# Kernel tuning notes

Measured on AMD Instinct MI355X. Metric: run time of the kernel, lower is better.

The kernel has to match this reference:

```python
import jax, jax.numpy as jnp
import numpy as np
from jax import lax

M_POINT = 1024
NSAMPLE = 16
GRASPNESS_THRESHOLD = 0.1
HMIN, HMAX = -0.02, 0.04  # cylinder height range (GraspNet CloudCrop)
RADII = (0.025, 0.05, 0.075, 0.1)
BIG = 1e10


def _fps(xyz, mask):
    """Masked furthest point sampling. xyz [N,3], mask [N] bool -> idx [M_POINT] int32.
    Masked-out points carry -BIG min-distance so they are never selected."""
    first = jnp.argmax(mask).astype(jnp.int32)  # first graspable point (ragged FPS start)
    dists = jnp.where(mask, BIG, -BIG)
    idxs = jnp.zeros((M_POINT,), jnp.int32).at[0].set(first)

    def body(i, carry):
        idxs, dists = carry
        last = xyz[idxs[i - 1]]
        d = jnp.sum((xyz - last) ** 2, axis=-1)
        dists = jnp.where(mask, jnp.minimum(dists, d), -BIG)
        nxt = jnp.argmax(dists).astype(jnp.int32)
        return idxs.at[i].set(nxt), dists

    idxs, _ = lax.fori_loop(1, M_POINT, body, (idxs, dists))
    return idxs


def _cylinder_crop(xyz_g, feat_g, rot, radius, w1, b1, w2, b2):
    """Cylinder query + group + shared MLP + maxpool.
    xyz_g [B,M,3], feat_g [B,M,C], rot [B,M,3,3] -> [B,M,256]."""
    B, M, _ = xyz_g.shape
    # offsets of candidate n relative to seed m, expressed in the seed's gripper frame
    diff = xyz_g[:, None, :, :] - xyz_g[:, :, None, :]          # [B,M(seed),M(cand),3]
    local = jnp.einsum('bmnj,bmji->bmni', diff, rot)            # rotate into approach frame
    along = local[..., 0]
    r2 = local[..., 1] ** 2 + local[..., 2] ** 2
    cond = (r2 < radius * radius) & (along > HMIN) & (along < HMAX)  # [B,M,M]
    # first NSAMPLE in-cylinder indices (ball-query semantics: pad with first hit)
    order = jnp.where(cond, jnp.arange(M)[None, None, :], M)
    sel = jnp.argsort(order, axis=-1)[..., :NSAMPLE].astype(jnp.int32)  # [B,M,NS]
    cnt = cond.sum(axis=-1)                                     # [B,M]
    fill = sel[..., :1]
    idx = jnp.where(jnp.arange(NSAMPLE)[None, None, :] < cnt[..., None], sel, fill)
    idx = jnp.where(cnt[..., None] > 0, idx, 0)
    grouped_xyz = jnp.take_along_axis(local, idx[..., None], axis=2) / radius  # [B,M,NS,3]
    grouped_feat = feat_g[jnp.arange(B)[:, None, None], idx]                    # [B,M,NS,C]
    g = jnp.concatenate([grouped_xyz, grouped_feat], axis=-1)                   # [B,M,NS,3+C]
    h = jax.nn.relu(jnp.einsum('bmnf,of->bmno', g, w1) + b1)
    h = jax.nn.relu(jnp.einsum('bmnf,of->bmno', h, w2) + b2)
    return h.max(axis=2)                                                        # [B,M,256]


def setup_inputs() -> dict:
    key = jax.random.key(0)
    ks = jax.random.split(key, 10)
    B, N, C = 4, 20000, 512
    return {
        'seed_xyz': jax.random.normal(ks[0], (B, N, 3), jnp.float32),
        'seed_features': jax.random.normal(ks[1], (B, C, N), jnp.float32),
        'objectness_score': jax.random.normal(ks[2], (B, 2, N), jnp.float32),
        'graspness_score': jax.random.uniform(ks[3], (B, N), jnp.float32),
        'grasp_top_views_rot': jax.random.normal(ks[4], (B, M_POINT, 3, 3), jnp.float32),
        'crop_w1': jax.random.normal(ks[5], (4, 256, 3 + C), jnp.float32) * 0.05,
        'crop_b1': jnp.zeros((4, 256), jnp.float32),
        'crop_w2': jax.random.normal(ks[6], (4, 256, 256), jnp.float32) * 0.05,
        'crop_b2': jnp.zeros((4, 256), jnp.float32),
        'fuse_w': jax.random.normal(ks[7], (256, 1024), jnp.float32) * 0.05,
        'fuse_b': jnp.zeros((256,), jnp.float32),
    }


def reference(seed_xyz, seed_features, objectness_score, graspness_score,
              grasp_top_views_rot, crop_w1, crop_b1, crop_w2, crop_b2,
              fuse_w, fuse_b):
    # graspable mask (per-point, data dependent)
    objectness_mask = jnp.argmax(objectness_score, axis=1) == 1       # [B,N]
    graspness_mask = graspness_score > GRASPNESS_THRESHOLD
    graspable_mask = objectness_mask & graspness_mask
    # masked FPS per sample, then gather
    idxs = jax.vmap(_fps)(seed_xyz, graspable_mask)                    # [B,M]
    xyz_g = jnp.take_along_axis(seed_xyz, idxs[:, :, None], axis=1)    # [B,M,3]
    feat = seed_features.transpose(0, 2, 1)                            # [B,N,C]
    feat_g = jnp.take_along_axis(feat, idxs[:, :, None], axis=1)       # [B,M,C]
    # multiscale cylinder crops
    feats = [_cylinder_crop(xyz_g, feat_g, grasp_top_views_rot, RADII[k],
                            crop_w1[k], crop_b1[k], crop_w2[k], crop_b2[k])
             for k in range(4)]
    cat = jnp.concatenate(feats, axis=-1)                              # [B,M,1024]
    fused = jnp.einsum('bmf,of->bom', cat, fuse_w) + fuse_b[None, :, None]  # [B,256,M]
    return fused
```

## Files before the change

### kernel.cpp

```cpp
#include <hip/hip_runtime.h>
#include <cstdint>
#include <cfloat>
#include <climits>

#define NPTS 20000
#define NB 4
#define MP 1024
#define CF 512
#define MAXCH 20
#define KFAST 10240
#define PPT 20

__constant__ float c_r2[4]  = { (float)(0.025*0.025), (float)(0.05*0.05),
                                (float)(0.075*0.075), (float)(0.1*0.1) };
__constant__ float c_rad[4] = { 0.025f, 0.05f, 0.075f, 0.1f };

#define DPP_XOR1   0xB1
#define DPP_XOR2   0x4E
#define DPP_HMIRR  0x141
#define DPP_MIRR   0x140
#define DPP_BC15   0x142
#define DPP_BC31   0x143

template<int CTRL>
__device__ __forceinline__ unsigned long long kmax_step(unsigned long long k)
{
    unsigned int lo = (unsigned int)k;
    unsigned int hi = (unsigned int)(k >> 32);
    unsigned int olo = (unsigned int)__builtin_amdgcn_update_dpp((int)lo, (int)lo, CTRL, 0xf, 0xf, false);
    unsigned int ohi = (unsigned int)__builtin_amdgcn_update_dpp((int)hi, (int)hi, CTRL, 0xf, 0xf, false);
    unsigned long long ok = ((unsigned long long)ohi << 32) | (unsigned long long)olo;
    return (ok > k) ? ok : k;
}

__global__ __launch_bounds__(1024)
void k_fps_compact(const float* __restrict__ xyz, const float* __restrict__ obj,
                   const float* __restrict__ grasp,
                   float* __restrict__ xc, float* __restrict__ yc,
                   float* __restrict__ zc, int* __restrict__ ci,
                   int* __restrict__ kv)
{
    const int b = blockIdx.x;
    const int tid = threadIdx.x;
    const int lane = tid & 63, wid = tid >> 6;
    const float* xb  = xyz   + (size_t)b * NPTS * 3;
    const float* ob0 = obj   + (size_t)b * 2 * NPTS;
    const float* ob1 = ob0 + NPTS;
    const float* gb  = grasp + (size_t)b * NPTS;
    float* xcb = xc + (size_t)b * 20480;
    float* ycb = yc + (size_t)b * 20480;
    float* zcb = zc + (size_t)b * 20480;
    int*   cib = ci + (size_t)b * 20480;

    __shared__ int sWaveCnt[16];

    int kbase = 0;
    for (int i = 0; i < MAXCH; ++i) {
        int n = i * MP + tid;
        bool msk = false; float x = 0.f, y = 0.f, z = 0.f;
        if (n < NPTS) {
            msk = (ob1[n] > ob0[n]) && (gb[n] > 0.1f);
            if (msk) { x = xb[n*3+0]; y = xb[n*3+1]; z = xb[n*3+2]; }
        }
        unsigned long long bal = __ballot(msk);
        if (lane == 0) sWaveCnt[wid] = __popcll(bal);
        __syncthreads();
        int pre = 0, tot = 0;
        for (int w = 0; w < 16; ++w) { int c = sWaveCnt[w]; tot += c; if (w < wid) pre += c; }
        if (msk) {
            int rank = kbase + pre + __popcll(bal & ((1ull << lane) - 1ull));
            xcb[rank] = x; ycb[rank] = y; zcb[rank] = z; cib[rank] = n;
        }
        kbase += tot;
        __syncthreads();
    }
    if (tid == 0) kv[b] = kbase;
}

__global__ __launch_bounds__(512, 2)
void k_fps_loop(const float* __restrict__ xyz, const int* __restrict__ kv,
                const float* __restrict__ xc, const float* __restrict__ yc,
                const float* __restrict__ zc, const int* __restrict__ ci,
                int* __restrict__ idxs, float* __restrict__ xyz_g)
{
    const int b = blockIdx.x;
    const int tid = threadIdx.x;
    const int lane = tid & 63, wid = tid >> 6;
    const float* xb  = xyz + (size_t)b * NPTS * 3;
    const float* xcb = xc + (size_t)b * 20480;
    const float* ycb = yc + (size_t)b * 20480;
    const float* zcb = zc + (size_t)b * 20480;
    const int*   cib = ci + (size_t)b * 20480;

    __shared__ float sXYZ[3 * KFAST];
    __shared__ int   s_sel[MP];
    __shared__ unsigned long long sKy[2][8];
    float* sX = sXYZ;
    float* sY = sXYZ + KFAST;
    float* sZ = sXYZ + 2 * KFAST;

    const int K = kv[b];

    if (K == 0) {
        for (int t = tid; t < MP; t += 512) {
            idxs[b*MP + t] = 0;
            xyz_g[((size_t)b*MP + t)*3 + 0] = xb[0];
            xyz_g[((size_t)b*MP + t)*3 + 1] = xb[1];
            xyz_g[((size_t)b*MP + t)*3 + 2] = xb[2];
        }
        return;
    }

    if (K <= KFAST) {
        for (int c = tid; c < KFAST; c += 512) {
            bool v = c < K;
            sX[c] = v ? xcb[c] : 0.f;
            sY[c] = v ? ycb[c] : 0.f;
            sZ[c] = v ? zcb[c] : 0.f;
        }
        __syncthreads();

        float px[PPT], py[PPT], pz[PPT], pd[PPT];
#pragma unroll
        for (int i = 0; i < PPT; ++i) {
            int c = tid + (i << 9);
            px[i] = sX[c]; py[i] = sY[c]; pz[i] = sZ[c];
            pd[i] = (c < K) ? 1e10f : -3.0e38f;
        }
        float lx = sX[0], ly = sY[0], lz = sZ[0];
        if (tid == 0) s_sel[0] = 0;

        for (int it = 1; it < MP; ++it) {
            const int p = it & 1;
#pragma unroll
            for (int i = 0; i < PPT; ++i) {
                float dx = px[i] - lx, dy = py[i] - ly, dz = pz[i] - lz;
                float d = __fadd_rn(__fadd_rn(__fmul_rn(dx,dx), __fmul_rn(dy,dy)),
                                    __fmul_rn(dz,dz));
                pd[i] = fminf(pd[i], d);
            }
            float gv[5]; int gi[5];
#pragma unroll
            for (int g = 0; g < 5; ++g) {
                const int i0 = g * 4;
                bool t0 = pd[i0+1] > pd[i0+0];
                float v01 = t0 ? pd[i0+1] : pd[i0+0];
                int   i01 = t0 ? (i0+1) : (i0+0);
                bool t1 = pd[i0+3] > pd[i0+2];
                float v23 = t1 ? pd[i0+3] : pd[i0+2];
                int   i23 = t1 ? (i0+3) : (i0+2);
                bool t2 = v23 > v01;
                gv[g] = t2 ? v23 : v01;
                gi[g] = t2 ? i23 : i01;
            }
            bool tA = gv[1] > gv[0]; float vA = tA ? gv[1] : gv[0]; int iA = tA ? gi[1] : gi[0];
            bool tB = gv[3] > gv[2]; float vB = tB ? gv[3] : gv[2]; int iB = tB ? gi[3] : gi[2];
            bool tC = vB > vA;       float vC = tC ? vB : vA;       int iC = tC ? iB : iA;
            bool tD = gv[4] > vC;    float bv = tD ? gv[4] : vC;    int bi = tD ? gi[4] : iC;
            int bn = tid + (bi << 9);

            unsigned int ob = __float_as_uint(bv);
            unsigned int ord = (ob & 0x80000000u) ? ~ob : (ob | 0x80000000u);
            unsigned long long key = ((unsigned long long)ord << 32)
                                   | (unsigned int)(~bn);
            key = kmax_step<DPP_XOR1 >(key);
            key = kmax_step<DPP_XOR2 >(key);
            key = kmax_step<DPP_HMIRR>(key);
            key = kmax_step<DPP_MIRR >(key);
            key = kmax_step<DPP_BC15 >(key);
            key = kmax_step<DPP_BC31 >(key);
            if (lane == 63) sKy[p][wid] = key;
            __syncthreads();
            unsigned long long k2 = sKy[p][lane & 7];
            k2 = kmax_step<DPP_XOR1 >(k2);
            k2 = kmax_step<DPP_XOR2 >(k2);
            k2 = kmax_step<DPP_HMIRR>(k2);
            int n = ~((unsigned int)k2);
            lx = sX[n]; ly = sY[n]; lz = sZ[n];
            if (tid == 0) s_sel[it] = n;
        }
        __syncthreads();
        for (int t = tid; t < MP; t += 512) {
            int nc = s_sel[t];
            idxs[b*MP + t] = cib[nc];
            xyz_g[((size_t)b*MP + t)*3 + 0] = sX[nc];
            xyz_g[((size_t)b*MP + t)*3 + 1] = sY[nc];
            xyz_g[((size_t)b*MP + t)*3 + 2] = sZ[nc];
        }
        return;
    }

    {
        float* fD = sXYZ;
        for (int c = tid; c < K; c += 512) fD[c] = 1e10f;
        float lx = xcb[0], ly = ycb[0], lz = zcb[0];
        if (tid == 0) s_sel[0] = 0;
        __syncthreads();
        for (int it = 1; it < MP; ++it) {
            const int p = it & 1;
            float bv = -3.4e38f; int bn = 0;
            for (int c = tid; c < K; c += 512) {
                float dx = xcb[c] - lx, dy = ycb[c] - ly, dz = zcb[c] - lz;
                float d = __fadd_rn(__fadd_rn(__fmul_rn(dx,dx), __fmul_rn(dy,dy)),
                                    __fmul_rn(dz,dz));
                float nd = fminf(fD[c], d);
                fD[c] = nd;
                bool w = nd > bv;
                bn = w ? c : bn;
                bv = fmaxf(bv, nd);
            }
            unsigned int ob = __float_as_uint(bv);
            unsigned int ord = (ob & 0x80000000u) ? ~ob : (ob | 0x80000000u);
            unsigned long long key = ((unsigned long long)ord << 32)
                                   | (unsigned int)(~bn);
            key = kmax_step<DPP_XOR1 >(key);
            key = kmax_step<DPP_XOR2 >(key);
            key = kmax_step<DPP_HMIRR>(key);
            key = kmax_step<DPP_MIRR >(key);
            key = kmax_step<DPP_BC15 >(key);
            key = kmax_step<DPP_BC31 >(key);
            if (lane == 63) sKy[p][wid] = key;
            __syncthreads();
            unsigned long long k2 = sKy[p][lane & 7];
            k2 = kmax_step<DPP_XOR1 >(k2);
            k2 = kmax_step<DPP_XOR2 >(k2);
            k2 = kmax_step<DPP_HMIRR>(k2);
            int n = ~((unsigned int)k2);
            lx = xcb[n]; ly = ycb[n]; lz = zcb[n];
            if (tid == 0) s_sel[it] = n;
        }
        __syncthreads();
        for (int t = tid; t < MP; t += 512) {
            int nc = s_sel[t];
            idxs[b*MP + t] = cib[nc];
            xyz_g[((size_t)b*MP + t)*3 + 0] = xcb[nc];
            xyz_g[((size_t)b*MP + t)*3 + 1] = ycb[nc];
            xyz_g[((size_t)b*MP + t)*3 + 2] = zcb[nc];
        }
    }
}

__global__ void k_gather_feat(const float* __restrict__ sf, const int* __restrict__ idxs,
                              float* __restrict__ feat_g)
{
    int bm = blockIdx.x;
    int b = bm >> 10;
    int n = idxs[bm];
    const float* src = sf + (size_t)b*CF*NPTS + n;
    float* dst = feat_g + (size_t)bm*CF;
    for (int c = threadIdx.x; c < CF; c += 256) dst[c] = src[(size_t)c * NPTS];
}

__global__ void k_prep(const float* __restrict__ w1, const float* __restrict__ w2,
                       float* __restrict__ w2t, float* __restrict__ w1x)
{
    int k = blockIdx.x, cb = blockIdx.y*32, ob = blockIdx.z*32;
    int tx = threadIdx.x & 31, ty = threadIdx.x >> 5;
    __shared__ float t[32][33];
    for (int r = ty; r < 32; r += 8)
        t[r][tx] = w2[((size_t)k*256 + ob + r)*256 + cb + tx];
    __syncthreads();
    for (int r = ty; r < 32; r += 8)
        w2t[((size_t)k*256 + cb + r)*256 + ob + tx] = t[tx][r];
    if (blockIdx.y == 0 && blockIdx.z == 0) {
        int o = threadIdx.x;
        for (int d = 0; d < 3; ++d)
            w1x[(k*3 + d)*256 + o] = w1[((size_t)k*256 + o)*515 + d];
    }
}

__global__ __launch_bounds__(256)
void k_f1(const float* __restrict__ feat_g, const float* __restrict__ w1,
          const float* __restrict__ b1, float* __restrict__ F1)
{
    const int rt = blockIdx.x * 64;
    const int ot = blockIdx.y * 64;
    const int k  = blockIdx.z;
    const int tid = threadIdx.x;
    __shared__ float As[16][68];
    __shared__ float Bs[16][68];
    const int lr = tid >> 2;
    const int lc = (tid & 3) * 4;
    const int tr = (tid & 15) * 4;
    const int tc = (tid >> 4) * 4;
    float acc[4][4] = {};
    for (int kk = 0; kk < CF; kk += 16) {
        const float* ap = feat_g + (size_t)(rt + lr)*CF + kk + lc;
        As[lc+0][lr] = ap[0]; As[lc+1][lr] = ap[1];
        As[lc+2][lr] = ap[2]; As[lc+3][lr] = ap[3];
        const float* bp = w1 + (size_t)(k*256 + ot + lr)*515 + 3 + kk + lc;
        Bs[lc+0][lr] = bp[0]; Bs[lc+1][lr] = bp[1];
        Bs[lc+2][lr] = bp[2]; Bs[lc+3][lr] = bp[3];
        __syncthreads();
#pragma unroll
        for (int cc = 0; cc < 16; ++cc) {
            float a0=As[cc][tr+0], a1=As[cc][tr+1], a2=As[cc][tr+2], a3=As[cc][tr+3];
            float q0=Bs[cc][tc+0], q1=Bs[cc][tc+1], q2=Bs[cc][tc+2], q3=Bs[cc][tc+3];
            acc[0][0]+=a0*q0; acc[0][1]+=a0*q1; acc[0][2]+=a0*q2; acc[0][3]+=a0*q3;
            acc[1][0]+=a1*q0; acc[1][1]+=a1*q1; acc[1][2]+=a1*q2; acc[1][3]+=a1*q3;
            acc[2][0]+=a2*q0; acc[2][1]+=a2*q1; acc[2][2]+=a2*q2; acc[2][3]+=a2*q3;
            acc[3][0]+=a3*q0; acc[3][1]+=a3*q1; acc[3][2]+=a3*q2; acc[3][3]+=a3*q3;
        }
        __syncthreads();
    }
#pragma unroll
    for (int i = 0; i < 4; ++i)
#pragma unroll
        for (int j = 0; j < 4; ++j)
            F1[((size_t)k*4096 + rt+tr+i)*256 + ot+tc+j] = acc[i][j] + b1[k*256 + ot+tc+j];
}

__global__ __launch_bounds__(1024)
void k_nbr(const float* __restrict__ xyz_g, const float* __restrict__ rot,
           int* __restrict__ sel, float* __restrict__ lxyz, int* __restrict__ cnt)
{
    const int bm = blockIdx.x;
    const int b = bm >> 10;
    const int tid = threadIdx.x;
    const int lane = tid & 63, wid = tid >> 6;
    __shared__ float sR[9], sC[3];
    __shared__ int   sSel[4][16];
    __shared__ float sL[4][16][3];
    __shared__ int   sW[16];
    __shared__ int   sCnt[4];
    __shared__ float sFb[3];
    if (tid < 9) sR[tid] = rot[(size_t)bm*9 + tid];
    if (tid < 3) sC[tid] = xyz_g[(size_t)bm*3 + tid];
    __syncthreads();
    float x = xyz_g[((size_t)b*MP + tid)*3 + 0];
    float y = xyz_g[((size_t)b*MP + tid)*3 + 1];
    float z = xyz_g[((size_t)b*MP + tid)*3 + 2];
    float dx = x - sC[0], dy = y - sC[1], dz = z - sC[2];
    float l0 = __fadd_rn(__fadd_rn(__fmul_rn(dx,sR[0]), __fmul_rn(dy,sR[3])), __fmul_rn(dz,sR[6]));
    float l1 = __fadd_rn(__fadd_rn(__fmul_rn(dx,sR[1]), __fmul_rn(dy,sR[4])), __fmul_rn(dz,sR[7]));
    float l2 = __fadd_rn(__fadd_rn(__fmul_rn(dx,sR[2]), __fmul_rn(dy,sR[5])), __fmul_rn(dz,sR[8]));
    float r2 = __fadd_rn(__fmul_rn(l1,l1), __fmul_rn(l2,l2));
    bool basec = (l0 > -0.02f) && (l0 < 0.04f);
    if (tid == 0) { sFb[0]=l0; sFb[1]=l1; sFb[2]=l2; }
    for (int k = 0; k < 4; ++k) {
        bool c = basec && (r2 < c_r2[k]);
        unsigned long long bal = __ballot(c);
        if (lane == 0) sW[wid] = __popcll(bal);
        __syncthreads();
        int pre = 0, tot = 0;
        for (int w = 0; w < 16; ++w) { int cw = sW[w]; tot += cw; if (w < wid) pre += cw; }
        int rank = pre + __popcll(bal & ((1ull << lane) - 1ull));
        if (c && rank < 16) {
            sSel[k][rank] = tid;
            sL[k][rank][0] = l0; sL[k][rank][1] = l1; sL[k][rank][2] = l2;
        }
        if (tid == 0) sCnt[k] = min(tot, 16);
        __syncthreads();
    }
    if (tid < 64) {
        int k = tid >> 4, j = tid & 15;
        int ck = sCnt[k];
        int src = (j < ck) ? j : 0;
        int v; float a0, a1, a2;
        if (ck > 0) { v = sSel[k][src]; a0=sL[k][src][0]; a1=sL[k][src][1]; a2=sL[k][src][2]; }
        else        { v = 0; a0=sFb[0]; a1=sFb[1]; a2=sFb[2]; }
        size_t off = ((size_t)bm*4 + k)*16 + j;
        sel[off] = v;
        lxyz[off*3+0]=a0; lxyz[off*3+1]=a1; lxyz[off*3+2]=a2;
        if (j == 0) cnt[bm*4 + k] = (ck > 0) ? ck : 1;
    }
}

__global__ __launch_bounds__(256)
void k_mlp(const float* __restrict__ F1, const float* __restrict__ w1x,
           const float* __restrict__ w2t, const float* __restrict__ b2,
           const int* __restrict__ sel, const float* __restrict__ lxyz,
           const int* __restrict__ cnt, float* __restrict__ cat)
{
    const int gid = blockIdx.x;
    const int k = gid & 3;
    const int g0 = (gid >> 2) * 4;
    const int o = threadIdx.x;
    __shared__ float h1s[64][256];
    int u0 = cnt[(g0+0)*4 + k], u1 = cnt[(g0+1)*4 + k],
        u2 = cnt[(g0+2)*4 + k], u3 = cnt[(g0+3)*4 + k];
    int off1 = u0, off2 = u0+u1, off3 = off2+u2, tot = off3+u3;
    const float wx0 = w1x[(k*3+0)*256 + o];
    const float wx1 = w1x[(k*3+1)*256 + o];
    const float wx2 = w1x[(k*3+2)*256 + o];
    const float rad = c_rad[k];
    const int bbase = (g0 >> 10) * MP;
    for (int r = 0; r < tot; ++r) {
        int t = (r >= off1) + (r >= off2) + (r >= off3);
        int toff = (t==0) ? 0 : ((t==1) ? off1 : ((t==2) ? off2 : off3));
        int j = r - toff;
        int bmk = (g0 + t)*4 + k;
        int n = sel[(size_t)bmk*16 + j];
        float lx = lxyz[((size_t)bmk*16 + j)*3 + 0];
        float ly = lxyz[((size_t)bmk*16 + j)*3 + 1];
        float lz = lxyz[((size_t)bmk*16 + j)*3 + 2];
        float v = F1[((size_t)k*4096 + bbase + n)*256 + o];
        v += (lx/rad)*wx0 + (ly/rad)*wx1 + (lz/rad)*wx2;
        h1s[r][o] = fmaxf(v, 0.f);
    }
    __syncthreads();
    const float b2v = b2[k*256 + o];
    float m0=0.f, m1=0.f, m2=0.f, m3=0.f;
    const float* w2c = w2t + (size_t)k*65536 + o;
    for (int base = 0; base < tot; base += 4) {
        int r0 = base;
        int r1 = min(base+1, tot-1);
        int r2 = min(base+2, tot-1);
        int r3 = min(base+3, tot-1);
        float a0=0.f, a1=0.f, a2=0.f, a3=0.f;
        for (int c = 0; c < 256; c += 4) {
            float wA = w2c[(c+0)*256], wB = w2c[(c+1)*256];
            float wC = w2c[(c+2)*256], wD = w2c[(c+3)*256];
            float4 h;
            h = *(const float4*)&h1s[r0][c]; a0 += h.x*wA + h.y*wB + h.z*wC + h.w*wD;
            h = *(const float4*)&h1s[r1][c]; a1 += h.x*wA + h.y*wB + h.z*wC + h.w*wD;
            h = *(const float4*)&h1s[r2][c]; a2 += h.x*wA + h.y*wB + h.z*wC + h.w*wD;
            h = *(const float4*)&h1s[r3][c]; a3 += h.x*wA + h.y*wB + h.z*wC + h.w*wD;
        }
#pragma unroll
        for (int q = 0; q < 4; ++q) {
            int r = base + q;
            if (r < tot) {
                float a = (q==0) ? a0 : ((q==1) ? a1 : ((q==2) ? a2 : a3));
                int t = (r >= off1) + (r >= off2) + (r >= off3);
                float val = fmaxf(a + b2v, 0.f);
                if      (t==0) m0 = fmaxf(m0, val);
                else if (t==1) m1 = fmaxf(m1, val);
                else if (t==2) m2 = fmaxf(m2, val);
                else           m3 = fmaxf(m3, val);
            }
        }
    }
    cat[(size_t)(g0+0)*1024 + k*256 + o] = m0;
    cat[(size_t)(g0+1)*1024 + k*256 + o] = m1;
    cat[(size_t)(g0+2)*1024 + k*256 + o] = m2;
    cat[(size_t)(g0+3)*1024 + k*256 + o] = m3;
}

__global__ void k_transpose(const float* __restrict__ cat, float* __restrict__ catT)
{
    int bt = blockIdx.x;
    int b = bt >> 10;
    int t2 = bt & 1023;
    int mi = (t2 >> 5) * 32, fi = (t2 & 31) * 32;
    int tx = threadIdx.x & 31, ty = threadIdx.x >> 5;
    __shared__ float t[32][33];
    const float* src = cat + (size_t)b * 1048576;
    float* dst = catT + (size_t)b * 1048576;
    for (int r = ty; r < 32; r += 8) t[r][tx] = src[(size_t)(mi + r)*1024 + fi + tx];
    __syncthreads();
    for (int r = ty; r < 32; r += 8) dst[(size_t)(fi + r)*1024 + mi + tx] = t[tx][r];
}

__global__ __launch_bounds__(256)
void k_fuse(const float* __restrict__ catT, const float* __restrict__ fw,
            const float* __restrict__ fb, float* __restrict__ out)
{
    const int o0 = blockIdx.x * 4;
    const int b = blockIdx.y;
    const int m = threadIdx.x * 4;
    const float* ct = catT + (size_t)b * 1048576 + m;
    float4 a0 = {0,0,0,0}, a1 = a0, a2 = a0, a3 = a0;
    for (int f = 0; f < 1024; ++f) {
        const float4 cv = *(const float4*)(ct + (size_t)f*1024);
        float w0 = fw[(size_t)(o0+0)*1024 + f];
        float w1 = fw[(size_t)(o0+1)*1024 + f];
        float w2 = fw[(size_t)(o0+2)*1024 + f];
        float w3 = fw[(size_t)(o0+3)*1024 + f];
        a0.x += cv.x*w0; a0.y += cv.y*w0; a0.z += cv.z*w0; a0.w += cv.w*w0;
        a1.x += cv.x*w1; a1.y += cv.y*w1; a1.z += cv.z*w1; a1.w += cv.w*w1;
        a2.x += cv.x*w2; a2.y += cv.y*w2; a2.z += cv.z*w2; a2.w += cv.w*w2;
        a3.x += cv.x*w3; a3.y += cv.y*w3; a3.z += cv.z*w3; a3.w += cv.w*w3;
    }
#pragma unroll
    for (int q = 0; q < 4; ++q) {
        float bb = fb[o0+q];
        float4 r = (q==0) ? a0 : ((q==1) ? a1 : ((q==2) ? a2 : a3));
        r.x += bb; r.y += bb; r.z += bb; r.w += bb;
        *(float4*)&out[((size_t)b*256 + o0 + q)*1024 + m] = r;
    }
}

extern "C" void kernel_launch(void* const* d_in, const int* in_sizes, int n_in,
                              void* d_out, int out_size, void* d_ws, size_t ws_size,
                              hipStream_t stream)
{
    const float* seed_xyz      = (const float*)d_in[0];
    const float* seed_features = (const float*)d_in[1];
    const float* objectness    = (const float*)d_in[2];
    const float* graspness     = (const float*)d_in[3];
    const float* rot           = (const float*)d_in[4];
    const float* w1            = (const float*)d_in[5];
    const float* b1            = (const float*)d_in[6];
    const float* w2            = (const float*)d_in[7];
    const float* b2            = (const float*)d_in[8];
    const float* fw            = (const float*)d_in[9];
    const float* fb            = (const float*)d_in[10];
    float* out = (float*)d_out;

    char* ws = (char*)d_ws;
    size_t off = 0;
    int*   idxs   = (int*)(ws + off);  off += 16u<<10;
    float* xyz_g  = (float*)(ws + off); off += 48u<<10;
    float* feat_g = (float*)(ws + off); off += 8u<<20;
    float* F1     = (float*)(ws + off); off += 16u<<20;
    float* w2t    = (float*)(ws + off); off += 1u<<20;
    float* w1x    = (float*)(ws + off); off += 64u<<10;
    int*   sel    = (int*)(ws + off);   off += 1u<<20;
    int*   cnt    = (int*)(ws + off);   off += 64u<<10;
    float* lxyz   = (float*)(ws + off); off += 3u<<20;
    float* cat    = (float*)(ws + off); off += 16u<<20;
    float* catT   = (float*)(ws + off); off += 16u<<20;

    float* xc = cat;
    float* yc = cat + 4*20480;
    float* zc = cat + 8*20480;
    int*   ci = (int*)(cat + 12*20480);
    int*   kv = (int*)((char*)w1x + 32768);

    k_fps_compact<<<NB, 1024, 0, stream>>>(seed_xyz, objectness, graspness,
                                           xc, yc, zc, ci, kv);
    k_fps_loop<<<NB, 512, 0, stream>>>(seed_xyz, kv, xc, yc, zc, ci, idxs, xyz_g);
    k_prep<<<dim3(4,8,8), 256, 0, stream>>>(w1, w2, w2t, w1x);
    k_gather_feat<<<NB*MP, 256, 0, stream>>>(seed_features, idxs, feat_g);
    k_f1<<<dim3(64,4,4), 256, 0, stream>>>(feat_g, w1, b1, F1);
    k_nbr<<<NB*MP, 1024, 0, stream>>>(xyz_g, rot, sel, lxyz, cnt);
    k_mlp<<<4096, 256, 0, stream>>>(F1, w1x, w2t, b2, sel, lxyz, cnt, cat);
    k_transpose<<<4096, 256, 0, stream>>>(cat, catT);
    k_fuse<<<dim3(64,4), 256, 0, stream>>>(catT, fw, fb, out);
}
```

Before: 1.725 ms.

## Use packed f32 math in FPS fast path and split argmax into max-then-index

The fast-path FPS loop now keeps point coordinates as float pairs and computes squared distances with v_pk_add/v_pk_mul, halving the VALU instruction count for the distance update. The argmax reduction changes from 64-bit key DPP reductions to a float-only max reduction, followed by an LDS atomicMin to find the smallest index holding that max. This cuts reduction work but adds a second barrier per iteration and an atomic. The -x offset via add keeps the rounding identical to the previous subtract.

```diff
diff --git a/kernel.cpp b/kernel.cpp
--- a/kernel.cpp
+++ b/kernel.cpp
@@ -9,7 +9,7 @@
 #define CF 512
 #define MAXCH 20
 #define KFAST 10240
-#define PPT 20
+#define PPAIR 10
 
 __constant__ float c_r2[4]  = { (float)(0.025*0.025), (float)(0.05*0.05),
                                 (float)(0.075*0.075), (float)(0.1*0.1) };
@@ -21,6 +21,23 @@
 #define DPP_MIRR   0x140
 #define DPP_BC15   0x142
 #define DPP_BC31   0x143
+
+typedef float v2f __attribute__((ext_vector_type(2)));
+
+__device__ __forceinline__ v2f pk_add(v2f a, v2f b){
+    v2f d; asm("v_pk_add_f32 %0, %1, %2" : "=v"(d) : "v"(a), "v"(b)); return d;
+}
+__device__ __forceinline__ v2f pk_mul(v2f a, v2f b){
+    v2f d; asm("v_pk_mul_f32 %0, %1, %2" : "=v"(d) : "v"(a), "v"(b)); return d;
+}
+
+template<int CTRL>
+__device__ __forceinline__ float fmax_dpp(float m)
+{
+    int mi = __float_as_int(m);
+    int oi = __builtin_amdgcn_update_dpp(mi, mi, CTRL, 0xf, 0xf, false);
+    return fmaxf(m, __int_as_float(oi));
+}
 
 template<int CTRL>
 __device__ __forceinline__ unsigned long long kmax_step(unsigned long long k)
@@ -95,6 +112,8 @@
     __shared__ float sXYZ[3 * KFAST];
     __shared__ int   s_sel[MP];
     __shared__ unsigned long long sKy[2][8];
+    __shared__ float sMax[2][8];
+    __shared__ int   sWinc[2];
     float* sX = sXYZ;
     float* sY = sXYZ + KFAST;
     float* sZ = sXYZ + 2 * KFAST;
@@ -118,66 +137,82 @@
             sY[c] = v ? ycb[c] : 0.f;
             sZ[c] = v ? zcb[c] : 0.f;
         }
-        __syncthreads();
-
-        float px[PPT], py[PPT], pz[PPT], pd[PPT];
-#pragma unroll
-        for (int i = 0; i < PPT; ++i) {
-            int c = tid + (i << 9);
-            px[i] = sX[c]; py[i] = sY[c]; pz[i] = sZ[c];
-            pd[i] = (c < K) ? 1e10f : -3.0e38f;
-        }
-        float lx = sX[0], ly = sY[0], lz = sZ[0];
-        if (tid == 0) s_sel[0] = 0;
+        if (tid == 0) { s_sel[0] = 0; sWinc[0] = 0x7fffffff; sWinc[1] = 0x7fffffff; }
+        __syncthreads();
+
+        v2f px2[PPAIR], py2[PPAIR], pz2[PPAIR], pd2[PPAIR];
+#pragma unroll
+        for (int i = 0; i < PPAIR; ++i) {
+            int c0 = tid + ((2*i) << 9);
+            int c1 = c0 + 512;
+            px2[i].x = sX[c0]; px2[i].y = sX[c1];
+            py2[i].x = sY[c0]; py2[i].y = sY[c1];
+            pz2[i].x = sZ[c0]; pz2[i].y = sZ[c1];
+            pd2[i].x = (c0 < K) ? 1e10f : -3.0e38f;
+            pd2[i].y = (c1 < K) ? 1e10f : -3.0e38f;
+            asm volatile("" : "+v"(px2[i]), "+v"(py2[i]), "+v"(pz2[i]));
+        }
+        v2f nlx2, nly2, nlz2;
+        {
+            float lx = sX[0], ly = sY[0], lz = sZ[0];
+            nlx2.x = nlx2.y = -lx; nly2.x = nly2.y = -ly; nlz2.x = nlz2.y = -lz;
+        }
 
         for (int it = 1; it < MP; ++it) {
             const int p = it & 1;
 #pragma unroll
-            for (int i = 0; i < PPT; ++i) {
-                float dx = px[i] - lx, dy = py[i] - ly, dz = pz[i] - lz;
-                float d = __fadd_rn(__fadd_rn(__fmul_rn(dx,dx), __fmul_rn(dy,dy)),
-                                    __fmul_rn(dz,dz));
-                pd[i] = fminf(pd[i], d);
+            for (int i = 0; i < PPAIR; ++i) {
+                v2f dx = pk_add(px2[i], nlx2);
+                v2f dy = pk_add(py2[i], nly2);
+                v2f dz = pk_add(pz2[i], nlz2);
+                v2f s  = pk_add(pk_add(pk_mul(dx,dx), pk_mul(dy,dy)), pk_mul(dz,dz));
+                pd2[i].x = fminf(pd2[i].x, s.x);
+                pd2[i].y = fminf(pd2[i].y, s.y);
             }
-            float gv[5]; int gi[5];
-#pragma unroll
-            for (int g = 0; g < 5; ++g) {
-                const int i0 = g * 4;
-                bool t0 = pd[i0+1] > pd[i0+0];
-                float v01 = t0 ? pd[i0+1] : pd[i0+0];
-                int   i01 = t0 ? (i0+1) : (i0+0);
-                bool t1 = pd[i0+3] > pd[i0+2];
-                float v23 = t1 ? pd[i0+3] : pd[i0+2];
-                int   i23 = t1 ? (i0+3) : (i0+2);
-                bool t2 = v23 > v01;
-                gv[g] = t2 ? v23 : v01;
-                gi[g] = t2 ? i23 : i01;
+            float q0 = fmaxf(pd2[0].x, pd2[0].y);
+            float q1 = fmaxf(pd2[1].x, pd2[1].y);
+            float q2 = fmaxf(pd2[2].x, pd2[2].y);
+            float q3 = fmaxf(pd2[3].x, pd2[3].y);
+            float q4 = fmaxf(pd2[4].x, pd2[4].y);
+            float q5 = fmaxf(pd2[5].x, pd2[5].y);
+            float q6 = fmaxf(pd2[6].x, pd2[6].y);
+            float q7 = fmaxf(pd2[7].x, pd2[7].y);
+            float q8 = fmaxf(pd2[8].x, pd2[8].y);
+            float q9 = fmaxf(pd2[9].x, pd2[9].y);
+            float r0 = fmaxf(fmaxf(q0, q1), fmaxf(q2, q3));
+            float r1 = fmaxf(fmaxf(q4, q5), fmaxf(q6, q7));
+            float bv = fmaxf(fmaxf(r0, r1), fmaxf(q8, q9));
+
+            float wm = bv;
+            wm = fmax_dpp<DPP_XOR1 >(wm);
+            wm = fmax_dpp<DPP_XOR2 >(wm);
+            wm = fmax_dpp<DPP_HMIRR>(wm);
+            wm = fmax_dpp<DPP_MIRR >(wm);
+            wm = fmax_dpp<DPP_BC15 >(wm);
+            wm = fmax_dpp<DPP_BC31 >(wm);
+            if (lane == 63) sMax[p][wid] = wm;
+            __syncthreads();
+            float g = sMax[p][lane & 7];
+            g = fmax_dpp<DPP_XOR1 >(g);
+            g = fmax_dpp<DPP_XOR2 >(g);
+            g = fmax_dpp<DPP_HMIRR>(g);
+            if (tid == 0) sWinc[p ^ 1] = 0x7fffffff;
+            if (bv == g) {
+                int c = 0x7fffffff;
+#pragma unroll
+                for (int i = PPAIR - 1; i >= 0; --i) {
+                    if (pd2[i].y == g) c = tid + ((2*i+1) << 9);
+                    if (pd2[i].x == g) c = tid + ((2*i  ) << 9);
+                }
+                atomicMin(&sWinc[p], c);
             }
-            bool tA = gv[1] > gv[0]; float vA = tA ? gv[1] : gv[0]; int iA = tA ? gi[1] : gi[0];
-            bool tB = gv[3] > gv[2]; float vB = tB ? gv[3] : gv[2]; int iB = tB ? gi[3] : gi[2];
-            bool tC = vB > vA;       float vC = tC ? vB : vA;       int iC = tC ? iB : iA;
-            bool tD = gv[4] > vC;    float bv = tD ? gv[4] : vC;    int bi = tD ? gi[4] : iC;
-            int bn = tid + (bi << 9);
-
-            unsigned int ob = __float_as_uint(bv);
-            unsigned int ord = (ob & 0x80000000u) ? ~ob : (ob | 0x80000000u);
-            unsigned long long key = ((unsigned long long)ord << 32)
-                                   | (unsigned int)(~bn);
-            key = kmax_step<DPP_XOR1 >(key);
-            key = kmax_step<DPP_XOR2 >(key);
-            key = kmax_step<DPP_HMIRR>(key);
-            key = kmax_step<DPP_MIRR >(key);
-            key = kmax_step<DPP_BC15 >(key);
-            key = kmax_step<DPP_BC31 >(key);
-            if (lane == 63) sKy[p][wid] = key;
             __syncthreads();
-            unsigned long long k2 = sKy[p][lane & 7];
-            k2 = kmax_step<DPP_XOR1 >(k2);
-            k2 = kmax_step<DPP_XOR2 >(k2);
-            k2 = kmax_step<DPP_HMIRR>(k2);
-            int n = ~((unsigned int)k2);
-            lx = sX[n]; ly = sY[n]; lz = sZ[n];
+            int n = sWinc[p];
             if (tid == 0) s_sel[it] = n;
+            float nx = sX[n], ny = sY[n], nz = sZ[n];
+            nlx2.x = nlx2.y = -nx;
+            nly2.x = nly2.y = -ny;
+            nlz2.x = nlz2.y = -nz;
         }
         __syncthreads();
         for (int t = tid; t < MP; t += 512) {
```

Measured after the change: 1.771 ms. +2.6%, slower.
